# Performance work log

Hardware: AMD Instinct MI355X
Metric: run time of the kernel (lower is better)

The kernel has to match this reference:

```python
import jax, jax.numpy as jnp
import numpy as np

N = 4_000_000

def setup_inputs() -> dict:
    key = jax.random.key(0)
    k1, k2 = jax.random.split(key)
    scaling_raw = jax.random.normal(k1, (N, 3), dtype=jnp.float32) * 0.5 - 3.0  # log-scales
    rotation = jax.random.normal(k2, (N, 4), dtype=jnp.float32)
    return {"scaling_raw": scaling_raw, "rotation": rotation}

def build_rotation(r):
    # r: (N,4) unnormalized quaternion (w,x,y,z)
    q = r / jnp.linalg.norm(r, axis=-1, keepdims=True)
    w, x, y, z = q[:, 0], q[:, 1], q[:, 2], q[:, 3]
    R = jnp.stack([
        1 - 2 * (y * y + z * z), 2 * (x * y - w * z),     2 * (x * z + w * y),
        2 * (x * y + w * z),     1 - 2 * (x * x + z * z), 2 * (y * z - w * x),
        2 * (x * z - w * y),     2 * (y * z + w * x),     1 - 2 * (x * x + y * y),
    ], axis=-1).reshape(-1, 3, 3)
    return R

def reference(scaling_raw, rotation):
    scaling_modifier = 1.0
    s = scaling_modifier * jnp.exp(scaling_raw)  # (N,3)
    R = build_rotation(rotation)                  # (N,3,3)
    L = R * s[:, None, :]                         # R @ diag(s)
    cov = jnp.einsum('nij,nkj->nik', L, L)        # L @ L^T, (N,3,3)
    # strip_symmetric: upper triangle [00,01,02,11,12,22]
    symm = jnp.stack([cov[:, 0, 0], cov[:, 0, 1], cov[:, 0, 2],
                      cov[:, 1, 1], cov[:, 1, 2], cov[:, 2, 2]], axis=-1)
    return symm
```

## Files before the change

kernel.cpp:

```cpp
#include <hip/hip_runtime.h>


__device__ __forceinline__ void cov6(float w, float x, float y, float z,
                                     float s0, float s1, float s2,
                                     float* __restrict__ c) {
    float inv = rsqrtf(w * w + x * x + y * y + z * z);
    w *= inv; x *= inv; y *= inv; z *= inv;
    float xx = x * x, yy = y * y, zz = z * z;
    float xy = x * y, xz = x * z, yz = y * z;
    float wx = w * x, wy = w * y, wz = w * z;
    float L00 = (1.f - 2.f * (yy + zz)) * s0, L01 = 2.f * (xy - wz) * s1, L02 = 2.f * (xz + wy) * s2;
    float L10 = 2.f * (xy + wz) * s0, L11 = (1.f - 2.f * (xx + zz)) * s1, L12 = 2.f * (yz - wx) * s2;
    float L20 = 2.f * (xz - wy) * s0, L21 = 2.f * (yz + wx) * s1, L22 = (1.f - 2.f * (xx + yy)) * s2;
    c[0] = L00 * L00 + L01 * L01 + L02 * L02;
    c[1] = L00 * L10 + L01 * L11 + L02 * L12;
    c[2] = L00 * L20 + L01 * L21 + L02 * L22;
    c[3] = L10 * L10 + L11 * L11 + L12 * L12;
    c[4] = L10 * L20 + L11 * L21 + L12 * L22;
    c[5] = L20 * L20 + L21 * L21 + L22 * L22;
}

__global__ __launch_bounds__(256) void gauss_cov4_kernel(
    const float4* __restrict__ sr4,
    const float4* __restrict__ rot,
    float4* __restrict__ out4,
    const float* __restrict__ sr,
    float* __restrict__ out,
    int n)
{
    int t = blockIdx.x * 256 + threadIdx.x;
    long long g = (long long)t * 4;
    if (g + 3 < n) {
        float4 a = sr4[3 * (size_t)t];
        float4 b = sr4[3 * (size_t)t + 1];
        float4 d = sr4[3 * (size_t)t + 2];
        float4 q0 = rot[g], q1 = rot[g + 1], q2 = rot[g + 2], q3 = rot[g + 3];

        float e0  = __expf(a.x), e1  = __expf(a.y), e2  = __expf(a.z);
        float e3  = __expf(a.w), e4  = __expf(b.x), e5  = __expf(b.y);
        float e6  = __expf(b.z), e7  = __expf(b.w), e8  = __expf(d.x);
        float e9  = __expf(d.y), e10 = __expf(d.z), e11 = __expf(d.w);

        float c[24];
        cov6(q0.x, q0.y, q0.z, q0.w, e0, e1, e2, c + 0);
        cov6(q1.x, q1.y, q1.z, q1.w, e3, e4, e5, c + 6);
        cov6(q2.x, q2.y, q2.z, q2.w, e6, e7, e8, c + 12);
        cov6(q3.x, q3.y, q3.z, q3.w, e9, e10, e11, c + 18);

        float4* o = out4 + 6 * (size_t)t;
        #pragma unroll
        for (int j = 0; j < 6; ++j)
            o[j] = make_float4(c[4 * j], c[4 * j + 1], c[4 * j + 2], c[4 * j + 3]);
    } else if (g < n) {
        for (long long i = g; i < n; ++i) {
            float4 q = rot[i];
            float e0 = __expf(sr[3 * i]), e1 = __expf(sr[3 * i + 1]), e2 = __expf(sr[3 * i + 2]);
            float c[6];
            cov6(q.x, q.y, q.z, q.w, e0, e1, e2, c);
            #pragma unroll
            for (int j = 0; j < 6; ++j) out[6 * i + j] = c[j];
        }
    }
}

extern "C" void kernel_launch(void* const* d_in, const int* in_sizes, int n_in,
                              void* d_out, int out_size, void* d_ws, size_t ws_size,
                              hipStream_t stream) {
    const float*  sr  = (const float*)d_in[0];
    const float4* rot = (const float4*)d_in[1];
    float* out = (float*)d_out;
    int n = in_sizes[0] / 3;

    int nthreads = (n + 3) / 4;
    int grid = (nthreads + 255) / 256;
    gauss_cov4_kernel<<<grid, 256, 0, stream>>>(
        (const float4*)sr, rot, (float4*)out, sr, out, n);
}
```

Before: 193.2 us.

## Stage inputs and outputs through LDS for fully coalesced float4 transfers

New measurement: 182.5 us. -5.6%, faster.

```diff
diff --git a/kernel.cpp b/kernel.cpp
--- a/kernel.cpp
+++ b/kernel.cpp
@@ -1,5 +1,13 @@
 #include <hip/hip_runtime.h>
 
+
+#define TPB 256
+#define GPB 512
+#define SC_SLOTS 384
+#define ROT_SLOTS 512
+#define OUT_SLOTS 768
+
+typedef float f32x4 __attribute__((ext_vector_type(4)));
 
 __device__ __forceinline__ void cov6(float w, float x, float y, float z,
                                      float s0, float s1, float s2,
@@ -20,59 +28,77 @@
     c[5] = L20 * L20 + L21 * L21 + L22 * L22;
 }
 
-__global__ __launch_bounds__(256) void gauss_cov4_kernel(
+__global__ __launch_bounds__(TPB, 8) void gauss_cov_lds(
     const float4* __restrict__ sr4,
-    const float4* __restrict__ rot,
+    const float4* __restrict__ rot4,
     float4* __restrict__ out4,
-    const float* __restrict__ sr,
-    float* __restrict__ out,
     int n)
 {
-    int t = blockIdx.x * 256 + threadIdx.x;
-    long long g = (long long)t * 4;
-    if (g + 3 < n) {
-        float4 a = sr4[3 * (size_t)t];
-        float4 b = sr4[3 * (size_t)t + 1];
-        float4 d = sr4[3 * (size_t)t + 2];
-        float4 q0 = rot[g], q1 = rot[g + 1], q2 = rot[g + 2], q3 = rot[g + 3];
+    __shared__ float4 lds[SC_SLOTS + ROT_SLOTS];
+    const int tid = threadIdx.x;
 
-        float e0  = __expf(a.x), e1  = __expf(a.y), e2  = __expf(a.z);
-        float e3  = __expf(a.w), e4  = __expf(b.x), e5  = __expf(b.y);
-        float e6  = __expf(b.z), e7  = __expf(b.w), e8  = __expf(d.x);
-        float e9  = __expf(d.y), e10 = __expf(d.z), e11 = __expf(d.w);
+    const long long sc_total  = (long long)n * 3 / 4;
+    const long long out_total = (long long)n * 6 / 4;
 
-        float c[24];
-        cov6(q0.x, q0.y, q0.z, q0.w, e0, e1, e2, c + 0);
-        cov6(q1.x, q1.y, q1.z, q1.w, e3, e4, e5, c + 6);
-        cov6(q2.x, q2.y, q2.z, q2.w, e6, e7, e8, c + 12);
-        cov6(q3.x, q3.y, q3.z, q3.w, e9, e10, e11, c + 18);
+    {
+        const long long sb = (long long)blockIdx.x * SC_SLOTS;
+        #pragma unroll
+        for (int k = 0; k < 2; ++k) {
+            int j = tid + k * TPB;
+            if (j < SC_SLOTS && sb + j < sc_total)
+                lds[j] = sr4[sb + j];
+        }
+        const long long rb = (long long)blockIdx.x * GPB;
+        #pragma unroll
+        for (int k = 0; k < 2; ++k) {
+            int j = tid + k * TPB;
+            int js = j ^ ((j >> 3) & 7);
+            if (rb + js < (long long)n)
+                lds[SC_SLOTS + j] = rot4[rb + js];
+        }
+    }
+    __syncthreads();
 
-        float4* o = out4 + 6 * (size_t)t;
-        #pragma unroll
-        for (int j = 0; j < 6; ++j)
-            o[j] = make_float4(c[4 * j], c[4 * j + 1], c[4 * j + 2], c[4 * j + 3]);
-    } else if (g < n) {
-        for (long long i = g; i < n; ++i) {
-            float4 q = rot[i];
-            float e0 = __expf(sr[3 * i]), e1 = __expf(sr[3 * i + 1]), e2 = __expf(sr[3 * i + 2]);
-            float c[6];
-            cov6(q.x, q.y, q.z, q.w, e0, e1, e2, c);
-            #pragma unroll
-            for (int j = 0; j < 6; ++j) out[6 * i + j] = c[j];
-        }
+    const float* ldsf = (const float*)lds;
+    float2 sa = *(const float2*)(ldsf + 6 * tid);
+    float2 sbv = *(const float2*)(ldsf + 6 * tid + 2);
+    float2 sc = *(const float2*)(ldsf + 6 * tid + 4);
+    int r0 = 2 * tid, r1 = 2 * tid + 1;
+    float4 q0 = lds[SC_SLOTS + (r0 ^ ((r0 >> 3) & 7))];
+    float4 q1 = lds[SC_SLOTS + (r1 ^ ((r1 >> 3) & 7))];
+    __syncthreads();
+
+    float e0 = __expf(sa.x), e1 = __expf(sa.y), e2 = __expf(sbv.x);
+    float e3 = __expf(sbv.y), e4 = __expf(sc.x), e5 = __expf(sc.y);
+    float c[12];
+    cov6(q0.x, q0.y, q0.z, q0.w, e0, e1, e2, c);
+    cov6(q1.x, q1.y, q1.z, q1.w, e3, e4, e5, c + 6);
+
+    float* outf = (float*)lds;
+    *(float4*)(outf + 12 * tid + 0) = make_float4(c[0], c[1], c[2],  c[3]);
+    *(float4*)(outf + 12 * tid + 4) = make_float4(c[4], c[5], c[6],  c[7]);
+    *(float4*)(outf + 12 * tid + 8) = make_float4(c[8], c[9], c[10], c[11]);
+    __syncthreads();
+
+    const long long ob = (long long)blockIdx.x * OUT_SLOTS;
+    const f32x4* ldsn = (const f32x4*)lds;
+    f32x4* outn = (f32x4*)out4;
+    #pragma unroll
+    for (int k = 0; k < 3; ++k) {
+        int j = tid + k * TPB;
+        if (ob + j < out_total)
+            __builtin_nontemporal_store(ldsn[j], &outn[ob + j]);
     }
 }
 
 extern "C" void kernel_launch(void* const* d_in, const int* in_sizes, int n_in,
                               void* d_out, int out_size, void* d_ws, size_t ws_size,
                               hipStream_t stream) {
-    const float*  sr  = (const float*)d_in[0];
-    const float4* rot = (const float4*)d_in[1];
-    float* out = (float*)d_out;
+    const float4* sr4  = (const float4*)d_in[0];
+    const float4* rot4 = (const float4*)d_in[1];
+    float4* out4 = (float4*)d_out;
     int n = in_sizes[0] / 3;
 
-    int nthreads = (n + 3) / 4;
-    int grid = (nthreads + 255) / 256;
-    gauss_cov4_kernel<<<grid, 256, 0, stream>>>(
-        (const float4*)sr, rot, (float4*)out, sr, out, n);
+    int grid = (int)(((long long)n + GPB - 1) / GPB);
+    gauss_cov_lds<<<grid, TPB, 0, stream>>>(sr4, rot4, out4, n);
 }
```
